# Optimization experiments

Measured on AMD Instinct MI355X. Metric: run time of the kernel, lower is better.

## Reference

```python
import jax, jax.numpy as jnp
import numpy as np

B, C, H, W = 8, 64, 64, 64  # module requires c == h == w due to view/permute quirk


def setup_inputs() -> dict:
    key = jax.random.key(0)
    ks = jax.random.split(key, 5)
    return {
        "x": jax.random.normal(ks[0], (B, C, H, W), dtype=jnp.float32),
        "w_qkv": jax.random.normal(ks[1], (3 * C, C), dtype=jnp.float32) * (1.0 / np.sqrt(C)),
        "b_qkv": jax.random.normal(ks[2], (3 * C,), dtype=jnp.float32) * 0.02,
        "w_out": jax.random.normal(ks[3], (C, C), dtype=jnp.float32) * (1.0 / np.sqrt(C)),
        "b_out": jax.random.normal(ks[4], (C,), dtype=jnp.float32) * 0.02,
    }


def reference(x, w_qkv, b_qkv, w_out, b_out):
    b, c, h, w = x.shape
    # 1x1 conv == channel matmul (norm='none' -> Identity, the only runnable branch)
    qkv = jnp.einsum('bchw,oc->bohw', x, w_qkv) + b_qkv[None, :, None, None]
    q, k, v = jnp.split(qkv, 3, axis=1)  # each (b, c, h, w)

    def flat(t):  # (b,c,h,w) -> (b, h*w, c), matches permute(0,2,3,1).view
        return t.transpose(0, 2, 3, 1).reshape(b, h * w, c)

    q, k, v = flat(q), flat(k), flat(v)
    scale = 1.0 / jnp.sqrt(jnp.asarray(c, dtype=x.dtype))
    scores = jax.nn.softmax(jnp.einsum('bqc,bkc->bqk', q, k) * scale, axis=-1)
    out = jnp.einsum('bqk,bkc->bqc', scores, v)  # (b, hw, c)
    # Faithfully replicate the original's view(b,c,h,w).permute(0,3,1,2) quirk
    out = out.reshape(b, c, h, w).transpose(0, 3, 1, 2)  # (b, w, c, h); needs c==h==w
    out = jnp.einsum('bchw,oc->bohw', out, w_out) + b_out[None, :, None, None]
    return out + x
```

## Files before the change

### kernel.cpp

```cpp
#include <hip/hip_runtime.h>
#include <hip/hip_bf16.h>
#include <stdint.h>

typedef unsigned short u16;
typedef __attribute__((ext_vector_type(8))) short bf16x8;
typedef __attribute__((ext_vector_type(4))) float f32x4;
typedef __attribute__((ext_vector_type(2))) float f32x2;
typedef __attribute__((ext_vector_type(4))) unsigned int u32x4;
typedef __attribute__((ext_vector_type(2))) unsigned int u32x2;

#define NTOK 4096
#define NT32 32

#if __has_builtin(__builtin_amdgcn_exp2f)
#define EXP2F __builtin_amdgcn_exp2f
#else
#define EXP2F exp2f
#endif

__device__ __forceinline__ f32x4 MFMA(bf16x8 a, bf16x8 b, f32x4 c) {
    return __builtin_amdgcn_mfma_f32_16x16x32_bf16(a, b, c, 0, 0, 0);
}

__device__ __forceinline__ uint32_t pk_bf16(float a, float b) {
    uint32_t d;
    asm("v_cvt_pk_bf16_f32 %0, %1, %2" : "=v"(d) : "v"(a), "v"(b));
    return d;
}

__device__ __forceinline__ void hilo_pack8(const float* v, bf16x8* h, bf16x8* l) {
    union { uint32_t u[4]; bf16x8 b; } H, L;
#pragma unroll
    for (int m = 0; m < 4; ++m) {
        const uint32_t ua = __float_as_uint(v[2*m]);
        const uint32_t ub = __float_as_uint(v[2*m+1]);
        const float la = v[2*m]   - __uint_as_float(ua & 0xffff0000u);
        const float lb = v[2*m+1] - __uint_as_float(ub & 0xffff0000u);
        H.u[m] = (ua >> 16) | (ub & 0xffff0000u);
        L.u[m] = (__float_as_uint(la) >> 16) | (__float_as_uint(lb) & 0xffff0000u);
    }
    *h = H.b; *l = L.b;
}

__global__ __launch_bounds__(256) void k_qkv(
    const float* __restrict__ x, const float* __restrict__ wqkv, const float* __restrict__ bqkv,
    u16* __restrict__ Qp, u16* __restrict__ Kp, u16* __restrict__ Vp)
{
    __shared__ float qt_lds[64 * 194];
    const int blk = blockIdx.x;
    const int b   = blk >> 6;
    const int tb  = (blk & 63) << 6;
    const int tid = threadIdx.x;
    const int lane = tid & 63;
    const int wv  = __builtin_amdgcn_readfirstlane(tid >> 6);
    const int r   = lane & 15;
    const int g   = lane >> 4;
    const int o0  = wv * 48;

    bf16x8 wh[3][2], wl[3][2];
#pragma unroll
    for (int oi = 0; oi < 3; ++oi)
#pragma unroll
        for (int ks = 0; ks < 2; ++ks) {
            const float* wp = wqkv + (size_t)(o0 + oi*16 + r) * 64 + ks*32 + g*8;
            float wv8[8];
            *(f32x4*)(wv8)     = *(const f32x4*)(wp);
            *(f32x4*)(wv8 + 4) = *(const f32x4*)(wp + 4);
            hilo_pack8(wv8, &wh[oi][ks], &wl[oi][ks]);
        }

    f32x4 acc[3][4];
#pragma unroll
    for (int oi = 0; oi < 3; ++oi)
#pragma unroll
        for (int tt = 0; tt < 4; ++tt) acc[oi][tt] = 0.f;

#pragma unroll
    for (int tt = 0; tt < 4; ++tt) {
        bf16x8 xh[2], xl[2];
#pragma unroll
        for (int ks = 0; ks < 2; ++ks) {
            float xv[8];
#pragma unroll
            for (int j = 0; j < 8; ++j)
                xv[j] = x[(size_t)(b*64 + ks*32 + g*8 + j) * NTOK + tb + tt*16 + r];
            hilo_pack8(xv, &xh[ks], &xl[ks]);
        }
#pragma unroll
        for (int oi = 0; oi < 3; ++oi) {
            f32x4 a = acc[oi][tt];
            a = MFMA(wh[oi][0], xh[0], a);
            a = MFMA(wh[oi][1], xh[1], a);
            a = MFMA(wl[oi][0], xh[0], a);
            a = MFMA(wl[oi][1], xh[1], a);
            a = MFMA(wh[oi][0], xl[0], a);
            a = MFMA(wh[oi][1], xl[1], a);
            acc[oi][tt] = a;
        }
    }

#pragma unroll
    for (int oi = 0; oi < 3; ++oi)
#pragma unroll
        for (int tt = 0; tt < 4; ++tt)
#pragma unroll
            for (int i = 0; i < 4; ++i)
                qt_lds[(tt*16 + r) * 194 + o0 + oi*16 + g*4 + i] = acc[oi][tt][i];
    __syncthreads();

    const float SC = 0.18033688011112042f;

    {
        const int t = tid >> 2, c0 = (tid & 3) * 16;
        float v[16], bq[16];
#pragma unroll
        for (int m = 0; m < 8; ++m)
            *(f32x2*)(v + 2*m) = *(const f32x2*)&qt_lds[t*194 + c0 + 2*m];
#pragma unroll
        for (int m = 0; m < 4; ++m)
            *(f32x4*)(bq + 4*m) = *(const f32x4*)(bqkv + c0 + 4*m);
        u32x4 P0, P1;
#pragma unroll
        for (int m = 0; m < 4; ++m) {
            P0[m] = pk_bf16((v[2*m]   + bq[2*m]  ) * SC, (v[2*m+1] + bq[2*m+1]) * SC);
            P1[m] = pk_bf16((v[8+2*m] + bq[8+2*m]) * SC, (v[9+2*m] + bq[9+2*m]) * SC);
        }
        size_t base = ((size_t)(b * NTOK + tb + t)) * 64 + c0;
        *(u32x4*)(Qp + base)     = P0;
        *(u32x4*)(Qp + base + 8) = P1;
    }

#pragma unroll
    for (int uu = 0; uu < 2; ++uu) {
        const int u  = tid * 2 + uu;
        const int t  = u >> 3;
        const int ks = (u >> 2) & 1;
        const int gk = u & 3;
        const int cb0 = 64 + ks*32 + gk*8;
        float v[8];
#pragma unroll
        for (int m = 0; m < 4; ++m)
            *(f32x2*)(v + 2*m) = *(const f32x2*)&qt_lds[t*194 + cb0 + 2*m];
        u32x4 P;
#pragma unroll
        for (int m = 0; m < 4; ++m)
            P[m] = pk_bf16(v[2*m] + bqkv[cb0 + 2*m], v[2*m+1] + bqkv[cb0 + 2*m+1]);
        const int tg = tb + t;
        size_t kbase = (size_t)b * 262144 + ((size_t)(tg >> 4) * 2 + ks) * 512 + gk*128 + (t & 15) * 8;
        *(u32x4*)(Kp + kbase) = P;
    }

    {
        const int cb = (tid >> 4) & 3;
        const int r2 = tid & 15;
        const float bv = bqkv[128 + cb*16 + r2];
        const int T = (blk & 63) >> 1;
        const int halfb = blk & 1;
#pragma unroll
        for (int m = 0; m < 4; ++m) {
            const int tq = m * 4 + (tid >> 6);
            float v[4];
#pragma unroll
            for (int jj = 0; jj < 4; ++jj)
                v[jj] = qt_lds[(tq*4 + jj)*194 + 128 + cb*16 + r2] + bv;
            const int t = tq * 4;
            const int wtr = halfb*2 + (t >> 5);
            const int sti = (t >> 4) & 1;
            const int g2  = (t >> 2) & 3;
            u32x2 W;
            W[0] = pk_bf16(v[0], v[1]);
            W[1] = pk_bf16(v[2], v[3]);
            size_t vbase = (size_t)b * 262144 +
                           (((size_t)T * 4 + wtr) * 4 + cb) * 512 + (g2*16 + r2) * 8 + sti * 4;
            *(u32x2*)(Vp + vbase) = W;
        }
    }
}

__global__ __launch_bounds__(256, 2) void k_attn(
    const u16* __restrict__ Qp, const u16* __restrict__ Kp, const u16* __restrict__ Vp,
    const float* __restrict__ wout, const float* __restrict__ bout,
    const float* __restrict__ x, float* __restrict__ out)
{
    __shared__ float larr[4][32];
    __shared__ float otbuf[2][32 * 67];
    const int hw  = blockIdx.x;
    const int b   = hw & 7;
    const int rest = hw >> 3;
    const int qt  = rest >> 1;
    const int wq  = rest & 1;
    const int tid = threadIdx.x;
    const int lane = tid & 63;
    const int wt2 = tid >> 6;
    const int r   = lane & 15;
    const int g   = lane >> 4;
    const int row0 = qt * 64 + wq * 32;

    bf16x8 qh[2][2];
#pragma unroll
    for (int rt = 0; rt < 2; ++rt) {
        const size_t qoff = ((size_t)(b * NTOK + row0 + rt*16 + r)) * 64 + g * 8;
        qh[rt][0] = *(const bf16x8*)(Qp + qoff);
        qh[rt][1] = *(const bf16x8*)(Qp + qoff + 32);
    }

    const u16* kptr = Kp + (size_t)b * 262144 + wt2 * 2048 + (size_t)lane * 8;
    const u16* vptr = Vp + (size_t)b * 262144 + wt2 * 2048 + (size_t)lane * 8;

    bf16x8 ONES;
#pragma unroll
    for (int j = 0; j < 8; ++j) ONES[j] = (short)0x3F80;

    f32x4 oacc[2][4];
#pragma unroll
    for (int rt = 0; rt < 2; ++rt)
#pragma unroll
        for (int cb = 0; cb < 4; ++cb) oacc[rt][cb] = 0.f;
    f32x4 lacc[2];
    lacc[0] = 0.f; lacc[1] = 0.f;

    for (int T = 0; T < NT32; ++T) {
        bf16x8 kc[2][2];
#pragma unroll
        for (int sti = 0; sti < 2; ++sti)
#pragma unroll
            for (int ks = 0; ks < 2; ++ks)
                kc[sti][ks] = *(const bf16x8*)(kptr + sti*1024 + ks*512);
        bf16x8 vf[4];
#pragma unroll
        for (int cb = 0; cb < 4; ++cb)
            vf[cb] = *(const bf16x8*)(vptr + cb*512);
        kptr += 8192;
        vptr += 8192;

        f32x4 s[2][2];
        __builtin_amdgcn_s_setprio(1);
#pragma unroll
        for (int rt = 0; rt < 2; ++rt)
#pragma unroll
            for (int sti = 0; sti < 2; ++sti) {
                f32x4 a = {0.f, 0.f, 0.f, 0.f};
                a = MFMA(kc[sti][0], qh[rt][0], a);
                a = MFMA(kc[sti][1], qh[rt][1], a);
                s[rt][sti] = a;
            }
        __builtin_amdgcn_s_setprio(0);

#pragma unroll
        for (int rt = 0; rt < 2; ++rt) {
            float p[8];
#pragma unroll
            for (int sti = 0; sti < 2; ++sti)
#pragma unroll
                for (int i = 0; i < 4; ++i)
                    p[sti*4 + i] = EXP2F(s[rt][sti][i]);
            union { uint32_t u[4]; bf16x8 b; } PA;
#pragma unroll
            for (int m = 0; m < 4; ++m) PA.u[m] = pk_bf16(p[2*m], p[2*m+1]);
            __builtin_amdgcn_s_setprio(1);
#pragma unroll
            for (int cb = 0; cb < 4; ++cb)
                oacc[rt][cb] = MFMA(PA.b, vf[cb], oacc[rt][cb]);
            lacc[rt] = MFMA(PA.b, ONES, lacc[rt]);
            __builtin_amdgcn_s_setprio(0);
        }
    }

    if (r == 0) {
#pragma unroll
        for (int rt = 0; rt < 2; ++rt)
#pragma unroll
            for (int i = 0; i < 4; ++i)
                larr[wt2][rt*16 + g*4 + i] = lacc[rt][i];
    }

    if (wt2 < 2) {
        float* ob = otbuf[wt2];
#pragma unroll
        for (int rt = 0; rt < 2; ++rt)
#pragma unroll
            for (int cb = 0; cb < 4; ++cb)
#pragma unroll
                for (int i = 0; i < 4; ++i)
                    ob[(rt*16 + g*4 + i)*67 + cb*16 + r] = oacc[rt][cb][i];
    }
    __syncthreads();
    if (wt2 >= 2) {
        float* ob = otbuf[wt2 - 2];
#pragma unroll
        for (int rt = 0; rt < 2; ++rt)
#pragma unroll
            for (int cb = 0; cb < 4; ++cb)
#pragma unroll
                for (int i = 0; i < 4; ++i)
                    ob[(rt*16 + g*4 + i)*67 + cb*16 + r] += oacc[rt][cb][i];
    }
    __syncthreads();

    const int rg  = wt2 & 1;
    const int ohf = wt2 >> 1;
    const int orow = rg*16 + r;
    const float ltot = larr[0][orow] + larr[1][orow] + larr[2][orow] + larr[3][orow];
    const float inv = 1.0f / ltot;
    bf16x8 oh_[2], ol_[2];
#pragma unroll
    for (int ks = 0; ks < 2; ++ks) {
        float ov[8];
#pragma unroll
        for (int j = 0; j < 8; ++j) {
            const int idx = orow*67 + ks*32 + g*8 + j;
            ov[j] = (otbuf[0][idx] + otbuf[1][idx]) * inv;
        }
        hilo_pack8(ov, &oh_[ks], &ol_[ks]);
    }
    f32x4 acc2[2];
#pragma unroll
    for (int ot = 0; ot < 2; ++ot) {
        bf16x8 wh2[2], wl2[2];
#pragma unroll
        for (int ks = 0; ks < 2; ++ks) {
            const float* wp = wout + (size_t)(ohf*32 + ot*16 + r) * 64 + ks*32 + g*8;
            float wv8[8];
            *(f32x4*)(wv8)     = *(const f32x4*)(wp);
            *(f32x4*)(wv8 + 4) = *(const f32x4*)(wp + 4);
            hilo_pack8(wv8, &wh2[ks], &wl2[ks]);
        }
        f32x4 a = {0.f, 0.f, 0.f, 0.f};
        a = MFMA(wh2[0], oh_[0], a);
        a = MFMA(wh2[1], oh_[1], a);
        a = MFMA(wl2[0], oh_[0], a);
        a = MFMA(wl2[1], oh_[1], a);
        a = MFMA(wh2[0], ol_[0], a);
        a = MFMA(wh2[1], ol_[1], a);
        acc2[ot] = a;
    }
#pragma unroll
    for (int ot = 0; ot < 2; ++ot)
#pragma unroll
        for (int i = 0; i < 4; ++i) {
            const int oo = ohf*32 + ot*16 + g*4 + i;
            const size_t xi = ((size_t)(b*64 + oo)) * NTOK + row0 + rg*16 + r;
            out[xi] = acc2[ot][i] + bout[oo] + x[xi];
        }
}

extern "C" void kernel_launch(void* const* d_in, const int* in_sizes, int n_in,
                              void* d_out, int out_size, void* d_ws, size_t ws_size,
                              hipStream_t stream)
{
    (void)in_sizes; (void)n_in; (void)out_size; (void)ws_size;
    const float* x    = (const float*)d_in[0];
    const float* wqkv = (const float*)d_in[1];
    const float* bqkv = (const float*)d_in[2];
    const float* wout = (const float*)d_in[3];
    const float* bout = (const float*)d_in[4];
    float* out = (float*)d_out;

    char* ws = (char*)d_ws;
    const size_t MB = 1024 * 1024;
    u16* Qp = (u16*)(ws);
    u16* Kp = (u16*)(ws + 4 * MB);
    u16* Vp = (u16*)(ws + 8 * MB);

    k_qkv<<<512, 256, 0, stream>>>(x, wqkv, bqkv, Qp, Kp, Vp);
    k_attn<<<1024, 256, 0, stream>>>(Qp, Kp, Vp, wout, bout, x, out);
}
```

Measured before the change: 61.85 us.

## Stage K/V tiles in LDS with async double buffering shared across query waves

The attention kernel now processes 64 query rows per block, with two query-row groups per block, instead of 32, and halves the grid. K/V tiles are copied into double-buffered LDS using global_load_lds so that two waves reuse each tile instead of each wave reading K/V from global memory. The split over the key axis drops from 4-way to 2-way per query group, which changes the LDS reduction and the output-projection mapping. This cuts global K/V traffic but adds a barrier every iteration, uses more LDS, and lowers the block count, which may reduce occupancy and latency hiding.

```diff
diff --git a/kernel.cpp b/kernel.cpp
--- a/kernel.cpp
+++ b/kernel.cpp
@@ -10,7 +10,7 @@
 typedef __attribute__((ext_vector_type(2))) unsigned int u32x2;
 
 #define NTOK 4096
-#define NT32 32
+#define NT64 64
 
 #if __has_builtin(__builtin_amdgcn_exp2f)
 #define EXP2F __builtin_amdgcn_exp2f
@@ -40,6 +40,12 @@
         L.u[m] = (__float_as_uint(la) >> 16) | (__float_as_uint(lb) & 0xffff0000u);
     }
     *h = H.b; *l = L.b;
+}
+
+__device__ __forceinline__ void async_copy16(void* lds_dst, const void* g_src) {
+    __builtin_amdgcn_global_load_lds(
+        (const __attribute__((address_space(1))) uint32_t*)g_src,
+        (__attribute__((address_space(3))) uint32_t*)lds_dst, 16, 0, 0);
 }
 
 __global__ __launch_bounds__(256) void k_qkv(
@@ -182,30 +188,51 @@
     const float* __restrict__ wout, const float* __restrict__ bout,
     const float* __restrict__ x, float* __restrict__ out)
 {
-    __shared__ float larr[4][32];
-    __shared__ float otbuf[2][32 * 67];
+    __shared__ __align__(16) char kv[2][16384];
+    __shared__ float otbuf[64 * 67];
+    __shared__ float larr[2][64];
     const int hw  = blockIdx.x;
     const int b   = hw & 7;
-    const int rest = hw >> 3;
-    const int qt  = rest >> 1;
-    const int wq  = rest & 1;
+    const int qb  = hw >> 3;
+    const int row0 = qb * 64;
     const int tid = threadIdx.x;
     const int lane = tid & 63;
-    const int wt2 = tid >> 6;
+    const int wv  = tid >> 6;
+    const int wq2 = wv >> 1;
+    const int wt  = wv & 1;
     const int r   = lane & 15;
     const int g   = lane >> 4;
-    const int row0 = qt * 64 + wq * 32;
 
     bf16x8 qh[2][2];
 #pragma unroll
     for (int rt = 0; rt < 2; ++rt) {
-        const size_t qoff = ((size_t)(b * NTOK + row0 + rt*16 + r)) * 64 + g * 8;
+        const size_t qoff = ((size_t)(b * NTOK + row0 + wq2*32 + rt*16 + r)) * 64 + g * 8;
         qh[rt][0] = *(const bf16x8*)(Qp + qoff);
         qh[rt][1] = *(const bf16x8*)(Qp + qoff + 32);
     }
 
-    const u16* kptr = Kp + (size_t)b * 262144 + wt2 * 2048 + (size_t)lane * 8;
-    const u16* vptr = Vp + (size_t)b * 262144 + wt2 * 2048 + (size_t)lane * 8;
+    const char* gK = (const char*)(Kp + (size_t)b * 262144);
+    const char* gV = (const char*)(Vp + (size_t)b * 262144);
+
+    auto stage = [&](int T, int buf) {
+        char* dst = kv[buf] + tid * 16;
+        const char* sK = gK + (size_t)T * 8192 + tid * 16;
+        const char* sV = gV + (size_t)T * 8192 + tid * 16;
+        async_copy16(dst,         sK);
+        async_copy16(dst + 4096,  sK + 4096);
+        async_copy16(dst + 8192,  sV);
+        async_copy16(dst + 12288, sV + 4096);
+    };
+
+    int koff[2][2], voff[4];
+#pragma unroll
+    for (int sti = 0; sti < 2; ++sti)
+#pragma unroll
+        for (int ks = 0; ks < 2; ++ks)
+            koff[sti][ks] = ((2*wt + sti)*2 + ks)*1024 + lane*16;
+#pragma unroll
+    for (int cb = 0; cb < 4; ++cb)
+        voff[cb] = 8192 + (wt*4 + cb)*1024 + lane*16;
 
     bf16x8 ONES;
 #pragma unroll
@@ -219,19 +246,25 @@
     f32x4 lacc[2];
     lacc[0] = 0.f; lacc[1] = 0.f;
 
-    for (int T = 0; T < NT32; ++T) {
+    stage(0, 0);
+    asm volatile("s_waitcnt vmcnt(0)" ::: "memory");
+    __syncthreads();
+    int cur = 0;
+
+    for (int T = 0; T < NT64; ++T) {
+        if (T + 1 < NT64) stage(T + 1, cur ^ 1);
+
+        const char* bufp = kv[cur];
         bf16x8 kc[2][2];
 #pragma unroll
         for (int sti = 0; sti < 2; ++sti)
 #pragma unroll
             for (int ks = 0; ks < 2; ++ks)
-                kc[sti][ks] = *(const bf16x8*)(kptr + sti*1024 + ks*512);
+                kc[sti][ks] = *(const bf16x8*)(bufp + koff[sti][ks]);
         bf16x8 vf[4];
 #pragma unroll
         for (int cb = 0; cb < 4; ++cb)
-            vf[cb] = *(const bf16x8*)(vptr + cb*512);
-        kptr += 8192;
-        vptr += 8192;
+            vf[cb] = *(const bf16x8*)(bufp + voff[cb]);
 
         f32x4 s[2][2];
         __builtin_amdgcn_s_setprio(1);
@@ -264,6 +297,10 @@
             lacc[rt] = MFMA(PA.b, ONES, lacc[rt]);
             __builtin_amdgcn_s_setprio(0);
         }
+
+        asm volatile("s_waitcnt vmcnt(0)" ::: "memory");
+        __syncthreads();
+        cur ^= 1;
     }
 
     if (r == 0) {
@@ -271,55 +308,47 @@
         for (int rt = 0; rt < 2; ++rt)
 #pragma unroll
             for (int i = 0; i < 4; ++i)
-                larr[wt2][rt*16 + g*4 + i] = lacc[rt][i];
-    }
-
-    if (wt2 < 2) {
-        float* ob = otbuf[wt2];
+                larr[wt][wq2*32 + rt*16 + g*4 + i] = lacc[rt][i];
+    }
+
+    if (wt == 0) {
 #pragma unroll
         for (int rt = 0; rt < 2; ++rt)
 #pragma unroll
             for (int cb = 0; cb < 4; ++cb)
 #pragma unroll
                 for (int i = 0; i < 4; ++i)
-                    ob[(rt*16 + g*4 + i)*67 + cb*16 + r] = oacc[rt][cb][i];
+                    otbuf[(wq2*32 + rt*16 + g*4 + i)*67 + cb*16 + r] = oacc[rt][cb][i];
     }
     __syncthreads();
-    if (wt2 >= 2) {
-        float* ob = otbuf[wt2 - 2];
+    if (wt == 1) {
 #pragma unroll
         for (int rt = 0; rt < 2; ++rt)
 #pragma unroll
             for (int cb = 0; cb < 4; ++cb)
 #pragma unroll
                 for (int i = 0; i < 4; ++i)
-                    ob[(rt*16 + g*4 + i)*67 + cb*16 + r] += oacc[rt][cb][i];
+                    otbuf[(wq2*32 + rt*16 + g*4 + i)*67 + cb*16 + r] += oacc[rt][cb][i];
     }
     __syncthreads();
 
-    const int rg  = wt2 & 1;
-    const int ohf = wt2 >> 1;
-    const int orow = rg*16 + r;
-    const float ltot = larr[0][orow] + larr[1][orow] + larr[2][orow] + larr[3][orow];
-    const float inv = 1.0f / ltot;
+    const int orow = wv*16 + r;
+    const float inv = 1.0f / (larr[0][orow] + larr[1][orow]);
     bf16x8 oh_[2], ol_[2];
 #pragma unroll
     for (int ks = 0; ks < 2; ++ks) {
         float ov[8];
 #pragma unroll
-        for (int j = 0; j < 8; ++j) {
-            const int idx = orow*67 + ks*32 + g*8 + j;
-            ov[j] = (otbuf[0][idx] + otbuf[1][idx]) * inv;
-        }
+        for (int j = 0; j < 8; ++j)
+            ov[j] = otbuf[orow*67 + ks*32 + g*8 + j] * inv;
         hilo_pack8(ov, &oh_[ks], &ol_[ks]);
     }
-    f32x4 acc2[2];
-#pragma unroll
-    for (int ot = 0; ot < 2; ++ot) {
+#pragma unroll
+    for (int ot = 0; ot < 4; ++ot) {
         bf16x8 wh2[2], wl2[2];
 #pragma unroll
         for (int ks = 0; ks < 2; ++ks) {
-            const float* wp = wout + (size_t)(ohf*32 + ot*16 + r) * 64 + ks*32 + g*8;
+            const float* wp = wout + (size_t)(ot*16 + r) * 64 + ks*32 + g*8;
             float wv8[8];
             *(f32x4*)(wv8)     = *(const f32x4*)(wp);
             *(f32x4*)(wv8 + 4) = *(const f32x4*)(wp + 4);
@@ -332,16 +361,13 @@
         a = MFMA(wl2[1], oh_[1], a);
         a = MFMA(wh2[0], ol_[0], a);
         a = MFMA(wh2[1], ol_[1], a);
-        acc2[ot] = a;
-    }
-#pragma unroll
-    for (int ot = 0; ot < 2; ++ot)
 #pragma unroll
         for (int i = 0; i < 4; ++i) {
-            const int oo = ohf*32 + ot*16 + g*4 + i;
-            const size_t xi = ((size_t)(b*64 + oo)) * NTOK + row0 + rg*16 + r;
-            out[xi] = acc2[ot][i] + bout[oo] + x[xi];
-        }
+            const int oo = ot*16 + g*4 + i;
+            const size_t xi = ((size_t)(b*64 + oo)) * NTOK + row0 + wv*16 + r;
+            out[xi] = a[i] + bout[oo] + x[xi];
+        }
+    }
 }
 
 extern "C" void kernel_launch(void* const* d_in, const int* in_sizes, int n_in,
@@ -363,5 +389,5 @@
     u16* Vp = (u16*)(ws + 8 * MB);
 
     k_qkv<<<512, 256, 0, stream>>>(x, wqkv, bqkv, Qp, Kp, Vp);
-    k_attn<<<1024, 256, 0, stream>>>(Qp, Kp, Vp, wout, bout, x, out);
-}
+    k_attn<<<512, 256, 0, stream>>>(Qp, Kp, Vp, wout, bout, x, out);
+}
```

Result: slower. 68.54 us (+10.8%).
